# Performance work log

Hardware: AMD Instinct MI355X
Metric: run time of the kernel (lower is better)

## Reference

```python
import jax, jax.numpy as jnp
import numpy as np

B, T, I, H, O = 32, 512, 256, 1024, 512
TRUNC = 500


def _lstm_layer(x_seq, W_ih, W_hh, b_ih, b_hh):
    # x_seq: [T, B, in]; W_ih: [4H, in]; W_hh: [4H, H]
    # Precompute input contribution for the whole sequence (big GEMM).
    xg = jnp.einsum('tbi,gi->tbg', x_seq, W_ih) + b_ih + b_hh  # [T, B, 4H]
    Hd = W_hh.shape[1]
    h0 = jnp.zeros((x_seq.shape[1], Hd), x_seq.dtype)

    def step(carry, xg_t):
        h, c = carry
        gates = xg_t + h @ W_hh.T  # [B, 4H]
        i, f, g, o = jnp.split(gates, 4, axis=-1)  # PyTorch gate order i,f,g,o
        c = jax.nn.sigmoid(f) * c + jax.nn.sigmoid(i) * jnp.tanh(g)
        h = jax.nn.sigmoid(o) * jnp.tanh(c)
        return (h, c), h

    (_, _), hs = jax.lax.scan(step, (h0, h0), xg)
    return hs  # [T, B, H]


def setup_inputs() -> dict:
    key = jax.random.key(0)
    ks = jax.random.split(key, 12)
    s = 1.0 / np.sqrt(H)  # PyTorch uniform(-1/sqrt(H), 1/sqrt(H)) scale
    u = lambda k, shp: jax.random.uniform(k, shp, jnp.float32, -s, s)
    return {
        'x': jax.random.normal(ks[0], (B, T, I), jnp.float32),
        'W_ih0': u(ks[1], (4 * H, I)),
        'W_hh0': u(ks[2], (4 * H, H)),
        'b_ih0': u(ks[3], (4 * H,)),
        'b_hh0': u(ks[4], (4 * H,)),
        'W_ih1': u(ks[5], (4 * H, H)),
        'W_hh1': u(ks[6], (4 * H, H)),
        'b_ih1': u(ks[7], (4 * H,)),
        'b_hh1': u(ks[8], (4 * H,)),
        'W_fc': u(ks[9], (O, H)),
        'b_fc': u(ks[10], (O,)),
    }


def reference(x, W_ih0, W_hh0, b_ih0, b_hh0, W_ih1, W_hh1, b_ih1, b_hh1, W_fc, b_fc):
    xs = jnp.transpose(x, (1, 0, 2))  # [T, B, I] (time-major for scan)
    h1 = _lstm_layer(xs, W_ih0, W_hh0, b_ih0, b_hh0)
    h2 = _lstm_layer(h1, W_ih1, W_hh1, b_ih1, b_hh1)
    out = jnp.transpose(h2, (1, 0, 2))[:, :TRUNC, :]  # [B, 500, H]
    return jnp.einsum('bth,oh->bto', out, W_fc) + b_fc
```

## Files before the change

### kernel.cpp

```cpp
#include <hip/hip_runtime.h>
#include <cstdint>
#include <cstddef>


#define NTHR 512

typedef _Float16 f16;
typedef _Float16 f16x8 __attribute__((ext_vector_type(8)));
typedef float f32x4 __attribute__((ext_vector_type(4)));
typedef unsigned long long u64;

namespace {
constexpr int kT = 512, kI = 256, kH = 1024, kO = 512, kTR = 500;
constexpr int kSteps = 500;
constexpr size_t kHalfSlot = 32768;
constexpr size_t kTagL0 = 0;
constexpr size_t kTagL1 = 4096;
constexpr size_t kH1Off = 16384;
constexpr size_t kH2Off = kH1Off + 503ull * 2 * kHalfSlot;
constexpr int kRowH = 1048;
constexpr int kRowX = 264;
constexpr int kLdsBytes = 2 * 16 * kRowH * 2 + 4 * 16 * 17 * 4;
}

__device__ __forceinline__ unsigned ld_tag(const void* p) {
  return __hip_atomic_load((const unsigned*)p, __ATOMIC_RELAXED,
                           __HIP_MEMORY_SCOPE_AGENT);
}
__device__ __forceinline__ void st_tag(void* p, unsigned v) {
  __hip_atomic_store((unsigned*)p, v, __ATOMIC_RELAXED,
                     __HIP_MEMORY_SCOPE_AGENT);
}
__device__ __forceinline__ void st_rec_u64(void* p, u64 v) {
  __hip_atomic_store((u64*)p, v, __ATOMIC_RELAXED, __HIP_MEMORY_SCOPE_AGENT);
}
__device__ __forceinline__ float sigmoid_f(float x) {
  return __builtin_amdgcn_rcpf(1.f + __expf(-x));
}
__device__ __forceinline__ float tanh_f(float x) {
  return 1.f - 2.f * __builtin_amdgcn_rcpf(1.f + __expf(2.f * x));
}
__device__ __forceinline__ f16x8 load8(const float* p) {
  f16x8 r;
#pragma unroll
  for (int j = 0; j < 8; ++j) r[j] = (f16)p[j];
  return r;
}
__device__ __forceinline__ u64 pack4(float h, int lg) {
  f16 hv = (f16)h;
  unsigned short us;
  __builtin_memcpy(&us, &hv, 2);
  unsigned own = us;
  unsigned o1 = __shfl_xor((int)own, 16);
  unsigned p32 = (lg & 1) ? ((o1 & 0xffffu) | (own << 16))
                          : ((own & 0xffffu) | (o1 << 16));
  unsigned o2 = (unsigned)__shfl_xor((int)p32, 32);
  return (lg & 2) ? ((u64)o2 | ((u64)p32 << 32))
                  : ((u64)p32 | ((u64)o2 << 32));
}

__global__ void __launch_bounds__(256, 1) lstm_init_kernel(char* ws) {
  const int gid = blockIdx.x * 256 + threadIdx.x;
  unsigned* f = (unsigned*)ws;
  if (gid < 4096) f[gid] = 0u;
  u64* r1 = (u64*)(ws + kH1Off);
  u64* r2 = (u64*)(ws + kH2Off);
  if (gid < 8192) { r1[gid] = 0ull; r2[gid] = 0ull; }
}

__global__ void __launch_bounds__(NTHR, 1) __attribute__((amdgpu_waves_per_eu(2)))
lstm_pipe_kernel(const float* __restrict__ x,
                 const float* __restrict__ Wih0, const float* __restrict__ Whh0,
                 const float* __restrict__ bih0, const float* __restrict__ bhh0,
                 const float* __restrict__ Wih1, const float* __restrict__ Whh1,
                 const float* __restrict__ bih1, const float* __restrict__ bhh1,
                 const float* __restrict__ Wfc, const float* __restrict__ bfc,
                 float* __restrict__ out, char* __restrict__ ws) {
  const int tid = threadIdx.x;
  const int bk = blockIdx.x;
  const int w = tid >> 6;
  const int lane = tid & 63;
  const int m = lane & 15;
  const int kg = lane >> 4;
  const int lg = lane >> 4;
  const int c = bk & 7, rho = bk >> 3;
  extern __shared__ char smem[];

  if (c < 2) {
    const int half = c;
    const int q = m >> 2, g = m & 3;
    const int uA = rho * 32 + 4 * w + q;
    const int uD = rho * 32 + 4 * w + lg;
    f16x8 whh[32], wih[8];
#pragma unroll
    for (int kc = 0; kc < 32; ++kc)
      whh[kc] = load8(Whh0 + (size_t)(g * kH + uA) * kH + kc * 32 + kg * 8);
#pragma unroll
    for (int kx = 0; kx < 8; ++kx)
      wih[kx] = load8(Wih0 + (size_t)(g * kH + uA) * kI + kx * 32 + kg * 8);
    float bias[4];
#pragma unroll
    for (int j = 0; j < 4; ++j) bias[j] = bih0[j * kH + uD] + bhh0[j * kH + uD];
    float cst = 0.f;
    f16* ldsH = (f16*)smem;
    f16* ldsX = (f16*)(smem + 16 * kRowH * 2);
    unsigned* tagMy = (unsigned*)(ws + kTagL0 + (size_t)half * 2048);
    const int xb = tid >> 5, xcol = (tid & 31) * 8;
    const int sb = tid >> 7, so = (tid & 127) * 8;

    for (int t = 1; t <= kSteps; ++t) {
      if (w == 7) {
        const unsigned tgt = (unsigned)(t - 1);
        const unsigned* tp = tagMy + (size_t)(lane & 31) * 16;
        bool done;
        do {
          done = __all((int)(ld_tag(tp) >= tgt));
          if (!done) __builtin_amdgcn_s_sleep(1);
        } while (!done);
      }
      {
        f16x8 xv = load8(x + ((size_t)(half * 16 + xb) * kT + (t - 1)) * kI + xcol);
        *(f16x8*)(ldsX + xb * kRowX + xcol) = xv;
      }
      __syncthreads();
      {
        const char* rec = ws + kH1Off + ((size_t)(t - 1) * 2 + half) * kHalfSlot;
        f16x8 h0 = *(const f16x8*)(rec + (size_t)tid * 16);
        f16x8 h1v = *(const f16x8*)(rec + (size_t)(tid + 512) * 16);
        f16x8 h2v = *(const f16x8*)(rec + (size_t)(tid + 1024) * 16);
        f16x8 h3v = *(const f16x8*)(rec + (size_t)(tid + 1536) * 16);
        *(f16x8*)(ldsH + (sb + 0) * kRowH + so) = h0;
        *(f16x8*)(ldsH + (sb + 4) * kRowH + so) = h1v;
        *(f16x8*)(ldsH + (sb + 8) * kRowH + so) = h2v;
        *(f16x8*)(ldsH + (sb + 12) * kRowH + so) = h3v;
      }
      __syncthreads();
      f32x4 acc = {0.f, 0.f, 0.f, 0.f};
#pragma unroll
      for (int kc = 0; kc < 32; ++kc) {
        f16x8 bf = *(const f16x8*)(ldsH + m * kRowH + kc * 32 + kg * 8);
        acc = __builtin_amdgcn_mfma_f32_16x16x32_f16(whh[kc], bf, acc, 0, 0, 0);
      }
#pragma unroll
      for (int kx = 0; kx < 8; ++kx) {
        f16x8 bf = *(const f16x8*)(ldsX + m * kRowX + kx * 32 + kg * 8);
        acc = __builtin_amdgcn_mfma_f32_16x16x32_f16(wih[kx], bf, acc, 0, 0, 0);
      }
      const float pi = acc[0] + bias[0], pf = acc[1] + bias[1];
      const float pg = acc[2] + bias[2], po = acc[3] + bias[3];
      cst = sigmoid_f(pf) * cst + sigmoid_f(pi) * tanh_f(pg);
      const float h = sigmoid_f(po) * tanh_f(cst);
      const u64 pk = pack4(h, lg);
      if (lane < 16) {
        st_rec_u64(ws + kH1Off + ((size_t)t * 2 + half) * kHalfSlot +
                       (size_t)lane * 2048 + (size_t)(rho * 32 + 4 * w) * 2,
                   pk);
        asm volatile("s_waitcnt vmcnt(0)" ::: "memory");
      }
      __syncthreads();
      if (tid == 0) st_tag(tagMy + (size_t)rho * 16, (unsigned)t);
    }

  } else if (c < 6) {
    const int half = c & 1;
    const int rank = rho + ((c >= 4) ? 32 : 0);
    const int u0 = rank * 16;
    const int rg = w & 3, kh = w >> 2;
    const int q = m >> 2, g = m & 3;
    const int uA = u0 + 4 * rg + q;
    const int uD = u0 + 4 * rg + lg;
    const float* WA = kh ? Whh1 : Wih1;
    f16x8 wa[32];
#pragma unroll
    for (int kc = 0; kc < 32; ++kc)
      wa[kc] = load8(WA + (size_t)(g * kH + uA) * kH + kc * 32 + kg * 8);
    float bias[4];
#pragma unroll
    for (int j = 0; j < 4; ++j) bias[j] = bih1[j * kH + uD] + bhh1[j * kH + uD];
    float cst = 0.f;
    f16* ldsH1 = (f16*)smem;
    f16* ldsH2 = (f16*)(smem + 16 * kRowH * 2);
    float* zone = (float*)(smem + 2 * 16 * kRowH * 2);
    unsigned* tagL0h = (unsigned*)(ws + kTagL0 + (size_t)half * 2048);
    unsigned* tagL1h = (unsigned*)(ws + kTagL1 + (size_t)half * 4096);
    const int sb = tid >> 7, so = (tid & 127) * 8;

    for (int t = 1; t <= kSteps; ++t) {
      if (w == 7) {
        const unsigned tgtB = (unsigned)(t - 1);
        const unsigned* tpB = tagL1h + (size_t)lane * 16;
        bool done;
        do {
          done = __all((int)(ld_tag(tpB) >= tgtB));
          if (!done) __builtin_amdgcn_s_sleep(1);
        } while (!done);
      }
      __syncthreads();
      {
        const char* r2 = ws + kH2Off + ((size_t)(t - 1) * 2 + half) * kHalfSlot;
        f16x8 b0 = *(const f16x8*)(r2 + (size_t)tid * 16);
        f16x8 b1 = *(const f16x8*)(r2 + (size_t)(tid + 512) * 16);
        f16x8 b2 = *(const f16x8*)(r2 + (size_t)(tid + 1024) * 16);
        f16x8 b3 = *(const f16x8*)(r2 + (size_t)(tid + 1536) * 16);
        if (w == 7) {
          const unsigned tgtA = (unsigned)t;
          const unsigned* tpA = tagL0h + (size_t)(lane & 31) * 16;
          bool done;
          do {
            done = __all((int)(ld_tag(tpA) >= tgtA));
            if (!done) __builtin_amdgcn_s_sleep(1);
          } while (!done);
        }
        *(f16x8*)(ldsH2 + (sb + 0) * kRowH + so) = b0;
        *(f16x8*)(ldsH2 + (sb + 4) * kRowH + so) = b1;
        *(f16x8*)(ldsH2 + (sb + 8) * kRowH + so) = b2;
        *(f16x8*)(ldsH2 + (sb + 12) * kRowH + so) = b3;
      }
      __syncthreads();
      if (kh == 1) {
        f32x4 acc = {0.f, 0.f, 0.f, 0.f};
#pragma unroll
        for (int kc = 0; kc < 32; ++kc) {
          f16x8 bf = *(const f16x8*)(ldsH2 + m * kRowH + kc * 32 + kg * 8);
          acc = __builtin_amdgcn_mfma_f32_16x16x32_f16(wa[kc], bf, acc, 0, 0, 0);
        }
#pragma unroll
        for (int j = 0; j < 4; ++j)
          zone[(rg * 16 + lg * 4 + j) * 17 + m] = acc[j];
      } else {
        const char* r1 = ws + kH1Off + ((size_t)t * 2 + half) * kHalfSlot;
        f16x8 a[8];
#pragma unroll
        for (int j = 0; j < 8; ++j)
          a[j] = *(const f16x8*)(r1 + ((size_t)(j * 256 + tid)) * 16);
#pragma unroll
        for (int j = 0; j < 8; ++j) {
          const int i = j * 256 + tid;
          *(f16x8*)(ldsH1 + (i >> 7) * kRowH + (i & 127) * 8) = a[j];
        }
      }
      __syncthreads();
      if (kh == 0) {
        f32x4 acc = {0.f, 0.f, 0.f, 0.f};
#pragma unroll
        for (int kc = 0; kc < 32; ++kc) {
          f16x8 bf = *(const f16x8*)(ldsH1 + m * kRowH + kc * 32 + kg * 8);
          acc = __builtin_amdgcn_mfma_f32_16x16x32_f16(wa[kc], bf, acc, 0, 0, 0);
        }
        const float pi = acc[0] + zone[(rg * 16 + lg * 4 + 0) * 17 + m] + bias[0];
        const float pf = acc[1] + zone[(rg * 16 + lg * 4 + 1) * 17 + m] + bias[1];
        const float pg = acc[2] + zone[(rg * 16 + lg * 4 + 2) * 17 + m] + bias[2];
        const float po = acc[3] + zone[(rg * 16 + lg * 4 + 3) * 17 + m] + bias[3];
        cst = sigmoid_f(pf) * cst + sigmoid_f(pi) * tanh_f(pg);
        const float h = sigmoid_f(po) * tanh_f(cst);
        const u64 pk = pack4(h, lg);
        if (lane < 16) {
          st_rec_u64(ws + kH2Off + ((size_t)t * 2 + half) * kHalfSlot +
                         (size_t)lane * 2048 + (size_t)(u0 + 4 * rg) * 2,
                     pk);
          asm volatile("s_waitcnt vmcnt(0)" ::: "memory");
        }
      }
      __syncthreads();
      if (tid == 0) st_tag(tagL1h + (size_t)rank * 16, (unsigned)t);
    }

  } else {
    const int half = c - 6;
    const int o0 = rho * 16;
    f16x8 wf[4];
#pragma unroll
    for (int i = 0; i < 4; ++i)
      wf[i] = load8(Wfc + (size_t)(o0 + m) * kH + (size_t)(w + 8 * i) * 32 + kg * 8);
    f16* ldsH = (f16*)smem;
    float* zone = (float*)(smem + 16 * kRowH * 2);
    unsigned* tagL1h = (unsigned*)(ws + kTagL1 + (size_t)half * 4096);
    const int sb = tid >> 7, so = (tid & 127) * 8;
    const int ob = lane >> 2, op = lane & 3;
    float4 bf4;
    if (w == 0) bf4 = *(const float4*)(bfc + o0 + op * 4);

    for (int t = 1; t <= kSteps; ++t) {
      if (w == 7) {
        const unsigned tgt = (unsigned)t;
        const unsigned* tp = tagL1h + (size_t)lane * 16;
        bool done;
        do {
          done = __all((int)(ld_tag(tp) >= tgt));
          if (!done) __builtin_amdgcn_s_sleep(1);
        } while (!done);
      }
      __syncthreads();
      {
        const char* r2 = ws + kH2Off + ((size_t)t * 2 + half) * kHalfSlot;
        f16x8 b0 = *(const f16x8*)(r2 + (size_t)tid * 16);
        f16x8 b1 = *(const f16x8*)(r2 + (size_t)(tid + 512) * 16);
        f16x8 b2 = *(const f16x8*)(r2 + (size_t)(tid + 1024) * 16);
        f16x8 b3 = *(const f16x8*)(r2 + (size_t)(tid + 1536) * 16);
        *(f16x8*)(ldsH + (sb + 0) * kRowH + so) = b0;
        *(f16x8*)(ldsH + (sb + 4) * kRowH + so) = b1;
        *(f16x8*)(ldsH + (sb + 8) * kRowH + so) = b2;
        *(f16x8*)(ldsH + (sb + 12) * kRowH + so) = b3;
      }
      __syncthreads();
      f32x4 acc = {0.f, 0.f, 0.f, 0.f};
#pragma unroll
      for (int i = 0; i < 4; ++i) {
        f16x8 bf = *(const f16x8*)(ldsH + m * kRowH + (w + 8 * i) * 32 + kg * 8);
        acc = __builtin_amdgcn_mfma_f32_16x16x32_f16(wf[i], bf, acc, 0, 0, 0);
      }
#pragma unroll
      for (int j = 0; j < 4; ++j)
        zone[(w * 16 + lg * 4 + j) * 17 + m] = acc[j];
      __syncthreads();
      if (w == 0) {
        float4 v;
#pragma unroll
        for (int jj = 0; jj < 4; ++jj) {
          float s = 0.f;
#pragma unroll
          for (int ww = 0; ww < 8; ++ww)
            s += zone[(ww * 16 + op * 4 + jj) * 17 + ob];
          ((float*)&v)[jj] = s + ((const float*)&bf4)[jj];
        }
        *(float4*)(out + ((size_t)(half * 16 + ob) * kTR + (t - 1)) * kO +
                   o0 + op * 4) = v;
      }
    }
  }
}

extern "C" void kernel_launch(void* const* d_in, const int* in_sizes, int n_in,
                              void* d_out, int out_size, void* d_ws,
                              size_t ws_size, hipStream_t stream) {
  const float* x    = (const float*)d_in[0];
  const float* Wih0 = (const float*)d_in[1];
  const float* Whh0 = (const float*)d_in[2];
  const float* bih0 = (const float*)d_in[3];
  const float* bhh0 = (const float*)d_in[4];
  const float* Wih1 = (const float*)d_in[5];
  const float* Whh1 = (const float*)d_in[6];
  const float* bih1 = (const float*)d_in[7];
  const float* bhh1 = (const float*)d_in[8];
  const float* Wfc  = (const float*)d_in[9];
  const float* bfc  = (const float*)d_in[10];
  float* out = (float*)d_out;
  char* ws   = (char*)d_ws;

  (void)hipFuncSetAttribute((const void*)lstm_pipe_kernel,
                            hipFuncAttributeMaxDynamicSharedMemorySize,
                            kLdsBytes);

  hipLaunchKernelGGL(lstm_init_kernel, dim3(128), dim3(256), 0, stream, ws);
  hipLaunchKernelGGL(lstm_pipe_kernel, dim3(256), dim3(NTHR), kLdsBytes,
                     stream, x, Wih0, Whh0, bih0, bhh0, Wih1, Whh1, bih1,
                     bhh1, Wfc, bfc, out, ws);
}
```

Baseline: 2.281 ms.

## Replace layer-0 block barriers with per-chunk LDS flags and streamed h loads

In the layer-0 recurrent loop, the single-wave global spin and two __syncthreads are replaced. Each wave now polls the producer tags only for the four h chunks it copies into LDS, then publishes a per-chunk LDS flag. Consumers wait on flags in groups of eight chunks, so MFMAs can start on partial data. The x-input contribution is computed first, straight from global memory, removing the x staging in LDS. This aims to overlap cross-block waiting with compute and cut barrier latency on the serial critical path. The cost is finer-grained polling and a correctness dependence on relaxed LDS flag ordering.

Measured after the change: 3.991 ms. 1.75x slower.

```diff
diff --git a/kernel.cpp b/kernel.cpp
--- a/kernel.cpp
+++ b/kernel.cpp
@@ -19,7 +19,6 @@
 constexpr size_t kH1Off = 16384;
 constexpr size_t kH2Off = kH1Off + 503ull * 2 * kHalfSlot;
 constexpr int kRowH = 1048;
-constexpr int kRowX = 264;
 constexpr int kLdsBytes = 2 * 16 * kRowH * 2 + 4 * 16 * 17 * 4;
 }
 
@@ -103,48 +102,58 @@
     for (int j = 0; j < 4; ++j) bias[j] = bih0[j * kH + uD] + bhh0[j * kH + uD];
     float cst = 0.f;
     f16* ldsH = (f16*)smem;
-    f16* ldsX = (f16*)(smem + 16 * kRowH * 2);
+    unsigned* ldsFlag = (unsigned*)(smem + 16 * kRowH * 2);
     unsigned* tagMy = (unsigned*)(ws + kTagL0 + (size_t)half * 2048);
-    const int xb = tid >> 5, xcol = (tid & 31) * 8;
-    const int sb = tid >> 7, so = (tid & 127) * 8;
+    const int sb2 = lane >> 2, pc = lane & 3;
+
+    if (tid < 32) ldsFlag[tid] = 0u;
+    __syncthreads();
 
     for (int t = 1; t <= kSteps; ++t) {
-      if (w == 7) {
+      f32x4 acc = {0.f, 0.f, 0.f, 0.f};
+      {
+        const float* xrow = x + ((size_t)(half * 16 + m) * kT + (t - 1)) * kI;
+#pragma unroll
+        for (int kx = 0; kx < 8; ++kx) {
+          f16x8 bf = load8(xrow + kx * 32 + kg * 8);
+          acc = __builtin_amdgcn_mfma_f32_16x16x32_f16(wih[kx], bf, acc, 0, 0, 0);
+        }
+      }
+      {
+        const char* rec = ws + kH1Off + ((size_t)(t - 1) * 2 + half) * kHalfSlot;
         const unsigned tgt = (unsigned)(t - 1);
-        const unsigned* tp = tagMy + (size_t)(lane & 31) * 16;
-        bool done;
-        do {
-          done = __all((int)(ld_tag(tp) >= tgt));
-          if (!done) __builtin_amdgcn_s_sleep(1);
-        } while (!done);
-      }
-      {
-        f16x8 xv = load8(x + ((size_t)(half * 16 + xb) * kT + (t - 1)) * kI + xcol);
-        *(f16x8*)(ldsX + xb * kRowX + xcol) = xv;
-      }
-      __syncthreads();
-      {
-        const char* rec = ws + kH1Off + ((size_t)(t - 1) * 2 + half) * kHalfSlot;
-        f16x8 h0 = *(const f16x8*)(rec + (size_t)tid * 16);
-        f16x8 h1v = *(const f16x8*)(rec + (size_t)(tid + 512) * 16);
-        f16x8 h2v = *(const f16x8*)(rec + (size_t)(tid + 1024) * 16);
-        f16x8 h3v = *(const f16x8*)(rec + (size_t)(tid + 1536) * 16);
-        *(f16x8*)(ldsH + (sb + 0) * kRowH + so) = h0;
-        *(f16x8*)(ldsH + (sb + 4) * kRowH + so) = h1v;
-        *(f16x8*)(ldsH + (sb + 8) * kRowH + so) = h2v;
-        *(f16x8*)(ldsH + (sb + 12) * kRowH + so) = h3v;
-      }
-      __syncthreads();
-      f32x4 acc = {0.f, 0.f, 0.f, 0.f};
-#pragma unroll
-      for (int kc = 0; kc < 32; ++kc) {
-        f16x8 bf = *(const f16x8*)(ldsH + m * kRowH + kc * 32 + kg * 8);
-        acc = __builtin_amdgcn_mfma_f32_16x16x32_f16(whh[kc], bf, acc, 0, 0, 0);
-      }
-#pragma unroll
-      for (int kx = 0; kx < 8; ++kx) {
-        f16x8 bf = *(const f16x8*)(ldsX + m * kRowX + kx * 32 + kg * 8);
-        acc = __builtin_amdgcn_mfma_f32_16x16x32_f16(wih[kx], bf, acc, 0, 0, 0);
+        for (int j = 0; j < 4; ++j) {
+          const int ch = 4 * w + j;
+          const unsigned* tp = tagMy + (size_t)ch * 16;
+          while (ld_tag(tp) < tgt) __builtin_amdgcn_s_sleep(1);
+          asm volatile("" ::: "memory");
+          f16x8 v = *(const f16x8*)(rec + (size_t)sb2 * 2048 + ch * 64 + pc * 16);
+          *(f16x8*)(ldsH + sb2 * kRowH + ch * 32 + pc * 8) = v;
+          asm volatile("s_waitcnt lgkmcnt(0)" ::: "memory");
+          if (lane == 0)
+            __hip_atomic_store(&ldsFlag[ch], (unsigned)t, __ATOMIC_RELAXED,
+                               __HIP_MEMORY_SCOPE_WORKGROUP);
+        }
+      }
+      {
+        const unsigned tgt = (unsigned)t;
+        for (int grp = 0; grp < 4; ++grp) {
+          bool done;
+          do {
+            unsigned fv = __hip_atomic_load(&ldsFlag[grp * 8 + (lane & 7)],
+                                            __ATOMIC_RELAXED,
+                                            __HIP_MEMORY_SCOPE_WORKGROUP);
+            done = __all((int)(fv >= tgt));
+            if (!done) __builtin_amdgcn_s_sleep(1);
+          } while (!done);
+          asm volatile("" ::: "memory");
+#pragma unroll
+          for (int k2 = 0; k2 < 8; ++k2) {
+            const int kc = grp * 8 + k2;
+            f16x8 bf = *(const f16x8*)(ldsH + m * kRowH + kc * 32 + kg * 8);
+            acc = __builtin_amdgcn_mfma_f32_16x16x32_f16(whh[kc], bf, acc, 0, 0, 0);
+          }
+        }
       }
       const float pi = acc[0] + bias[0], pf = acc[1] + bias[1];
       const float pg = acc[2] + bias[2], po = acc[3] + bias[3];
@@ -155,8 +164,8 @@
         st_rec_u64(ws + kH1Off + ((size_t)t * 2 + half) * kHalfSlot +
                        (size_t)lane * 2048 + (size_t)(rho * 32 + 4 * w) * 2,
                    pk);
-        asm volatile("s_waitcnt vmcnt(0)" ::: "memory");
-      }
+      }
+      asm volatile("s_waitcnt vmcnt(0)" ::: "memory");
       __syncthreads();
       if (tid == 0) st_tag(tagMy + (size_t)rho * 16, (unsigned)t);
     }
```

## Replace end-of-step barrier with LDS counter publish and double-buffer x tile

Applied to the files above, without the earlier changes.

In the layer-0 and layer-1 recurrent loops, the trailing __syncthreads before publishing the step tag is removed. Each wave now waits for its own stores and bumps a workgroup-scope LDS counter, and the last wave to arrive publishes the tag. The x input tile in LDS is double-buffered by step parity so the next step's x write cannot race with readers of the current one. This is meant to take a full block barrier off the serial recurrence's critical path, but it relies on relaxed atomics and per-wave vmcnt waits for memory ordering.

Measured after the change: 2.625 ms. +15.1%, slower.

```diff
diff --git a/kernel.cpp b/kernel.cpp
--- a/kernel.cpp
+++ b/kernel.cpp
@@ -20,7 +20,9 @@
 constexpr size_t kH2Off = kH1Off + 503ull * 2 * kHalfSlot;
 constexpr int kRowH = 1048;
 constexpr int kRowX = 264;
-constexpr int kLdsBytes = 2 * 16 * kRowH * 2 + 4 * 16 * 17 * 4;
+constexpr int kHBytes = 16 * kRowH * 2;
+constexpr int kXBytes = 16 * kRowX * 2;
+constexpr int kLdsBytes = 2 * kHBytes + 4 * 16 * 17 * 4 + 64;
 }
 
 __device__ __forceinline__ unsigned ld_tag(const void* p) {
@@ -103,10 +105,15 @@
     for (int j = 0; j < 4; ++j) bias[j] = bih0[j * kH + uD] + bhh0[j * kH + uD];
     float cst = 0.f;
     f16* ldsH = (f16*)smem;
-    f16* ldsX = (f16*)(smem + 16 * kRowH * 2);
+    f16* ldsX0 = (f16*)(smem + kHBytes);
+    f16* ldsX1 = (f16*)(smem + kHBytes + kXBytes);
+    unsigned* cnt = (unsigned*)(smem + kHBytes + 2 * kXBytes);
     unsigned* tagMy = (unsigned*)(ws + kTagL0 + (size_t)half * 2048);
     const int xb = tid >> 5, xcol = (tid & 31) * 8;
     const int sb = tid >> 7, so = (tid & 127) * 8;
+
+    if (tid == 0) cnt[0] = 0u;
+    __syncthreads();
 
     for (int t = 1; t <= kSteps; ++t) {
       if (w == 7) {
@@ -119,6 +126,7 @@
         } while (!done);
       }
       {
+        f16* ldsX = (t & 1) ? ldsX1 : ldsX0;
         f16x8 xv = load8(x + ((size_t)(half * 16 + xb) * kT + (t - 1)) * kI + xcol);
         *(f16x8*)(ldsX + xb * kRowX + xcol) = xv;
       }
@@ -141,10 +149,13 @@
         f16x8 bf = *(const f16x8*)(ldsH + m * kRowH + kc * 32 + kg * 8);
         acc = __builtin_amdgcn_mfma_f32_16x16x32_f16(whh[kc], bf, acc, 0, 0, 0);
       }
-#pragma unroll
-      for (int kx = 0; kx < 8; ++kx) {
-        f16x8 bf = *(const f16x8*)(ldsX + m * kRowX + kx * 32 + kg * 8);
-        acc = __builtin_amdgcn_mfma_f32_16x16x32_f16(wih[kx], bf, acc, 0, 0, 0);
+      {
+        const f16* ldsX = (t & 1) ? ldsX1 : ldsX0;
+#pragma unroll
+        for (int kx = 0; kx < 8; ++kx) {
+          f16x8 bf = *(const f16x8*)(ldsX + m * kRowX + kx * 32 + kg * 8);
+          acc = __builtin_amdgcn_mfma_f32_16x16x32_f16(wih[kx], bf, acc, 0, 0, 0);
+        }
       }
       const float pi = acc[0] + bias[0], pf = acc[1] + bias[1];
       const float pg = acc[2] + bias[2], po = acc[3] + bias[3];
@@ -155,10 +166,14 @@
         st_rec_u64(ws + kH1Off + ((size_t)t * 2 + half) * kHalfSlot +
                        (size_t)lane * 2048 + (size_t)(rho * 32 + 4 * w) * 2,
                    pk);
-        asm volatile("s_waitcnt vmcnt(0)" ::: "memory");
-      }
-      __syncthreads();
-      if (tid == 0) st_tag(tagMy + (size_t)rho * 16, (unsigned)t);
+      }
+      asm volatile("s_waitcnt vmcnt(0)" ::: "memory");
+      if (lane == 0) {
+        unsigned old = __hip_atomic_fetch_add(cnt, 1u, __ATOMIC_RELAXED,
+                                              __HIP_MEMORY_SCOPE_WORKGROUP);
+        if (old == 8u * (unsigned)t - 1u)
+          st_tag(tagMy + (size_t)rho * 16, (unsigned)t);
+      }
     }
 
   } else if (c < 6) {
@@ -179,11 +194,15 @@
     for (int j = 0; j < 4; ++j) bias[j] = bih1[j * kH + uD] + bhh1[j * kH + uD];
     float cst = 0.f;
     f16* ldsH1 = (f16*)smem;
-    f16* ldsH2 = (f16*)(smem + 16 * kRowH * 2);
-    float* zone = (float*)(smem + 2 * 16 * kRowH * 2);
+    f16* ldsH2 = (f16*)(smem + kHBytes);
+    float* zone = (float*)(smem + 2 * kHBytes);
+    unsigned* cnt = (unsigned*)(smem + 2 * kHBytes + 4 * 16 * 17 * 4);
     unsigned* tagL0h = (unsigned*)(ws + kTagL0 + (size_t)half * 2048);
     unsigned* tagL1h = (unsigned*)(ws + kTagL1 + (size_t)half * 4096);
     const int sb = tid >> 7, so = (tid & 127) * 8;
+
+    if (tid == 0) cnt[0] = 0u;
+    __syncthreads();
 
     for (int t = 1; t <= kSteps; ++t) {
       if (w == 7) {
@@ -258,11 +277,15 @@
           st_rec_u64(ws + kH2Off + ((size_t)t * 2 + half) * kHalfSlot +
                          (size_t)lane * 2048 + (size_t)(u0 + 4 * rg) * 2,
                      pk);
-          asm volatile("s_waitcnt vmcnt(0)" ::: "memory");
-        }
-      }
-      __syncthreads();
-      if (tid == 0) st_tag(tagL1h + (size_t)rank * 16, (unsigned)t);
+        }
+        asm volatile("s_waitcnt vmcnt(0)" ::: "memory");
+        if (lane == 0) {
+          unsigned old = __hip_atomic_fetch_add(cnt, 1u, __ATOMIC_RELAXED,
+                                                __HIP_MEMORY_SCOPE_WORKGROUP);
+          if (old == 4u * (unsigned)t - 1u)
+            st_tag(tagL1h + (size_t)rank * 16, (unsigned)t);
+        }
+      }
     }
 
   } else {
@@ -273,7 +296,7 @@
     for (int i = 0; i < 4; ++i)
       wf[i] = load8(Wfc + (size_t)(o0 + m) * kH + (size_t)(w + 8 * i) * 32 + kg * 8);
     f16* ldsH = (f16*)smem;
-    float* zone = (float*)(smem + 16 * kRowH * 2);
+    float* zone = (float*)(smem + kHBytes);
     unsigned* tagL1h = (unsigned*)(ws + kTagL1 + (size_t)half * 4096);
     const int sb = tid >> 7, so = (tid & 127) * 8;
     const int ob = lane >> 2, op = lane & 3;
```
